# Performance work log

Measured on AMD Instinct MI355X. Metric: run time of the kernel, lower is better.

Reference implementation:

```python
import jax, jax.numpy as jnp
import numpy as np

H = 256   # hidden_size
L = 6     # num_layers
IN = 128  # input_size
B = 128   # batch
T = 512   # seq_len


def setup_inputs() -> dict:
    key = jax.random.key(0)
    ks = jax.random.split(key, 9)
    s = 1.0 / np.sqrt(H)  # PyTorch LSTM init: U(-1/sqrt(H), 1/sqrt(H))
    x = jax.random.normal(ks[0], (B, T, IN), jnp.float32)
    h0 = jax.random.normal(ks[1], (L, B, H), jnp.float32)
    c0 = jax.random.normal(ks[2], (L, B, H), jnp.float32)
    w_ih0 = jax.random.uniform(ks[3], (4 * H, IN), jnp.float32, -s, s)
    w_ih = jax.random.uniform(ks[4], (L - 1, 4 * H, H), jnp.float32, -s, s)
    w_hh = jax.random.uniform(ks[5], (L, 4 * H, H), jnp.float32, -s, s)
    b_ih = jax.random.uniform(ks[6], (L, 4 * H), jnp.float32, -s, s)
    b_hh = jax.random.uniform(ks[7], (L, 4 * H), jnp.float32, -s, s)
    return {"x": x, "h0": h0, "c0": c0, "w_ih0": w_ih0, "w_ih": w_ih,
            "w_hh": w_hh, "b_ih": b_ih, "b_hh": b_hh}


def _lstm_layer(x, h0, c0, w_ih, w_hh, b):
    """One unidirectional LSTM layer. x: [B,T,Din] -> outputs [B,T,H], (hT, cT)."""
    # Precompute input contribution for all timesteps at once: [B,T,4H]
    xg = jnp.einsum('btd,gd->btg', x, w_ih) + b

    def step(carry, g_t):
        h, c = carry
        g = g_t + h @ w_hh.T  # [B,4H]
        i, f, gc, o = jnp.split(g, 4, axis=-1)  # PyTorch gate order i,f,g,o
        i = jax.nn.sigmoid(i)
        f = jax.nn.sigmoid(f)
        o = jax.nn.sigmoid(o)
        gc = jnp.tanh(gc)
        c = f * c + i * gc
        h = o * jnp.tanh(c)
        return (h, c), h

    (hT, cT), ys = jax.lax.scan(step, (h0, c0), jnp.swapaxes(xg, 0, 1))
    return jnp.swapaxes(ys, 0, 1), hT, cT


def reference(x, h0, c0, w_ih0, w_ih, w_hh, b_ih, b_hh):
    # Stacked 6-layer LSTM; fc / noop linear in the original is dead code.
    # Original returns state[0] (final hidden states, [L,B,H]) as float32.
    hs = []
    inp = x
    for l in range(L):
        wih_l = w_ih0 if l == 0 else w_ih[l - 1]
        b_l = b_ih[l] + b_hh[l]
        inp, hT, _ = _lstm_layer(inp, h0[l], c0[l], wih_l, w_hh[l], b_l)
        hs.append(hT)
    return jnp.stack(hs).astype(jnp.float32)  # [L, B, H]
```

## Files before the change

kernel.cpp:

```cpp
#include <hip/hip_runtime.h>

#define NLAYER 6
#define NB     128
#define NT     512
#define DIN    128
#define NH     256
#define NBLK   192
#define SLOT_U64 (NB*NH/4)

typedef __attribute__((ext_vector_type(8))) short short8;
typedef __attribute__((ext_vector_type(4))) float f32x4;
typedef unsigned long long u64;

__device__ __forceinline__ unsigned f2bf2(float lo, float hi){
  unsigned a = __float_as_uint(lo), b = __float_as_uint(hi);
  a = (a + 0x7fffu + ((a>>16)&1u)) >> 16;
  b = (b + 0x7fffu + ((b>>16)&1u)) >> 16;
  return a | (b<<16);
}
__device__ __forceinline__ u64 f2bf4(float a, float b, float c, float d){
  return (u64)f2bf2(a,b) | ((u64)f2bf2(c,d) << 32);
}
__device__ __forceinline__ short8 pack16(u64 lo, u64 hi){
  union { u64 u[2]; short8 v; } w; w.u[0]=lo; w.u[1]=hi; return w.v;
}
__device__ __forceinline__ short8 ld8f_frag(const float* p){
  f32x4 a = *(const f32x4*)p;
  f32x4 b = *(const f32x4*)(p+4);
  return pack16(f2bf4(a[0],a[1],a[2],a[3]), f2bf4(b[0],b[1],b[2],b[3]));
}

__device__ __forceinline__ float sigmf(float v){ return 1.0f/(1.0f + __expf(-v)); }
__device__ __forceinline__ float tanhfast(float v){
  v = fminf(fmaxf(v, -15.0f), 15.0f);
  float e = __expf(2.0f*v);
  return (e - 1.0f)/(e + 1.0f);
}

__device__ __forceinline__ int ld_flag(const int* p){
  return __hip_atomic_load(p, __ATOMIC_RELAXED, __HIP_MEMORY_SCOPE_AGENT);
}
__device__ __forceinline__ void st_flag(int* p, int v){
  __hip_atomic_store(p, v, __ATOMIC_RELAXED, __HIP_MEMORY_SCOPE_AGENT);
}
__device__ __forceinline__ u64 ring_ld(const u64* p){
  return __hip_atomic_load(p, __ATOMIC_RELAXED, __HIP_MEMORY_SCOPE_AGENT);
}
__device__ __forceinline__ void ring_st(u64* p, u64 v){
  __hip_atomic_store(p, v, __ATOMIC_RELAXED, __HIP_MEMORY_SCOPE_AGENT);
}

__device__ __forceinline__ void poll2(const int* tH, int needH,
                                      const int* tX, int needX, int lane){
  const int* tp = nullptr; int need = 0;
  if (lane < 16)               { tp = tH + lane;        need = needH; }
  else if (tX && lane < 32)    { tp = tX + (lane - 16); need = needX; }
  int guard = 0;
  for (;;){
    int v = tp ? ld_flag(tp) : 0x7fffffff;
    if (__ballot(v >= need) == ~0ull) break;
    __builtin_amdgcn_s_sleep(1);
    if (++guard > (1<<22)) break;
  }
  asm volatile("" ::: "memory");
}

__device__ __forceinline__ void stage_plane(const u64* __restrict__ src,
                                            u64* __restrict__ dst, int wv, int lane){
  const int r = lane >> 4, c = lane & 15;
  const u64* p = src + (size_t)(wv*4 + r)*64 + c*4;
  u64 v0 = ring_ld(p), v1 = ring_ld(p+1), v2 = ring_ld(p+2), v3 = ring_ld(p+3);
  u64* d = dst + (wv*4 + r)*66 + c*4;
  d[0] = v0; d[1] = v1; d[2] = v2; d[3] = v3;
}
__device__ __forceinline__ short8 lds_frag(const u64* __restrict__ buf, int row, int off){
  return *(const short8*)((const short*)buf + row*264 + off);
}

template<int NKX>
__device__ __forceinline__ void lstm_run(
    const float* __restrict__ x,  const float* __restrict__ h0,
    const float* __restrict__ c0, const float* __restrict__ wx,
    const float* __restrict__ wh, const float* __restrict__ bi,
    const float* __restrict__ bh, float* __restrict__ out,
    int* __restrict__ tags, int* __restrict__ acks,
    u64* __restrict__ ring, u64 (*ldsb)[1056],
    int Wv, int l, int bg, int s, int wv, int lane)
{
  constexpr int KIT  = NKX + 8;
  constexpr int KX   = NKX*32;
  constexpr bool HASX = (NKX == 8);
  const int l15  = lane & 15;
  const int quad = lane >> 4;
  const int bloc = bg*16 + l15;
  const int jcol = s*16 + quad*4;
  const int Wm   = Wv - 1;

  short8 A[4][KIT];
  #pragma unroll
  for (int q = 0; q < 4; ++q){
    const float* wrow_x = wx + (size_t)(q*NH + s*16 + l15)*KX;
    const float* wrow_h = wh + (size_t)(q*NH + s*16 + l15)*NH;
    #pragma unroll
    for (int kt = 0; kt < KIT; ++kt){
      int k0 = kt*32 + quad*8;
      A[q][kt] = (k0 < KX) ? ld8f_frag(wrow_x + k0)
                           : ld8f_frag(wrow_h + (k0 - KX));
    }
  }

  f32x4 bsv[4];
  #pragma unroll
  for (int q = 0; q < 4; ++q){
    f32x4 a = *(const f32x4*)(bi + q*NH + jcol);
    f32x4 b = *(const f32x4*)(bh + q*NH + jcol);
    bsv[q] = a + b;
  }
  float cc[4];
  {
    f32x4 cv = *(const f32x4*)(c0 + ((size_t)l*NB + bloc)*NH + jcol);
    cc[0]=cv[0]; cc[1]=cv[1]; cc[2]=cv[2]; cc[3]=cv[3];
  }

  int* tagOwn   = tags + (l*8 + bg)*16;
  const int* tagPrev = HASX ? tags + ((l-1)*8 + bg)*16 : nullptr;
  const int* ackOwn  = acks + (l*8 + bg)*16;
  int* ackPrevW = HASX ? acks + ((l-1)*8 + bg)*16 + s : nullptr;
  const u64* ringPrev = HASX ? ring + (size_t)(l-1)*Wv*SLOT_U64 : nullptr;
  u64*       ringOwn  = ring + (size_t)l*Wv*SLOT_U64;
  const bool lastL = (l == NLAYER-1);
  const bool wrap  = (Wv < NT);
  int ackmin = 0;

  for (int t = 0; t < NT; ++t){
    const int slot  = t & Wm;
    const int pslot = (t-1) & Wm;

    if (wrap && !lastL && t >= Wv){
      const int need = t - Wv + 1;
      if (ackmin < need){
        int v = 0, guard = 0;
        for (;;){
          v = (lane < 16) ? ld_flag(ackOwn + lane) : 0x7fffffff;
          if (__ballot(v >= need) == ~0ull) break;
          __builtin_amdgcn_s_sleep(1);
          if (++guard > (1<<22)) break;
        }
        int m = v;
        #pragma unroll
        for (int o = 8; o; o >>= 1) m = min(m, __shfl_xor(m, o));
        ackmin = __shfl(m, 0);
      }
    }

    short8 Bx[NKX];
    if constexpr (!HASX){
      const float* px = x + ((size_t)bloc*NT + t)*DIN + quad*8;
      #pragma unroll
      for (int k = 0; k < NKX; ++k) Bx[k] = ld8f_frag(px + k*32);
    }

    poll2(tagOwn, t, tagPrev, t+1, lane);

    u64* ldsX = ldsb[(t&1)*2 + 0];
    u64* ldsH = ldsb[(t&1)*2 + 1];
    if constexpr (HASX)
      stage_plane(ringPrev + (size_t)slot*SLOT_U64 + (size_t)bg*16*64, ldsX, wv, lane);
    if (t > 0)
      stage_plane(ringOwn + (size_t)pslot*SLOT_U64 + (size_t)bg*16*64, ldsH, wv, lane);
    __syncthreads();

    if (HASX && wrap && ((t & 7) == 7) && lane == 0) st_flag(ackPrevW, t+1);

    if constexpr (HASX){
      #pragma unroll
      for (int k = 0; k < NKX; ++k) Bx[k] = lds_frag(ldsX, l15, quad*8 + k*32);
    }
    short8 Bh[8];
    if (t == 0){
      const float* ph = h0 + ((size_t)l*NB + bloc)*NH + quad*8;
      #pragma unroll
      for (int k = 0; k < 8; ++k) Bh[k] = ld8f_frag(ph + k*32);
    } else {
      #pragma unroll
      for (int k = 0; k < 8; ++k) Bh[k] = lds_frag(ldsH, l15, quad*8 + k*32);
    }

    f32x4 a0 = {0,0,0,0}, a1 = {0,0,0,0}, a2 = {0,0,0,0}, a3 = {0,0,0,0};
    #pragma unroll
    for (int k = 0; k < NKX; ++k){
      a0 = __builtin_amdgcn_mfma_f32_16x16x32_bf16(A[0][k], Bx[k], a0, 0, 0, 0);
      a1 = __builtin_amdgcn_mfma_f32_16x16x32_bf16(A[1][k], Bx[k], a1, 0, 0, 0);
      a2 = __builtin_amdgcn_mfma_f32_16x16x32_bf16(A[2][k], Bx[k], a2, 0, 0, 0);
      a3 = __builtin_amdgcn_mfma_f32_16x16x32_bf16(A[3][k], Bx[k], a3, 0, 0, 0);
    }
    #pragma unroll
    for (int k = 0; k < 8; ++k){
      a0 = __builtin_amdgcn_mfma_f32_16x16x32_bf16(A[0][NKX+k], Bh[k], a0, 0, 0, 0);
      a1 = __builtin_amdgcn_mfma_f32_16x16x32_bf16(A[1][NKX+k], Bh[k], a1, 0, 0, 0);
      a2 = __builtin_amdgcn_mfma_f32_16x16x32_bf16(A[2][NKX+k], Bh[k], a2, 0, 0, 0);
      a3 = __builtin_amdgcn_mfma_f32_16x16x32_bf16(A[3][NKX+k], Bh[k], a3, 0, 0, 0);
    }

    float hv[4];
    #pragma unroll
    for (int r = 0; r < 4; ++r){
      float ig = sigmf(a0[r] + bsv[0][r]);
      float fg = sigmf(a1[r] + bsv[1][r]);
      float gv = tanhfast(a2[r] + bsv[2][r]);
      float og = sigmf(a3[r] + bsv[3][r]);
      float cn = fg*cc[r] + ig*gv;
      cc[r] = cn;
      hv[r] = og * tanhfast(cn);
    }

    ring_st(ringOwn + (size_t)slot*SLOT_U64 + (size_t)bloc*64 + s*4 + quad,
            f2bf4(hv[0], hv[1], hv[2], hv[3]));
    if (t == NT-1){
      f32x4 ov; ov[0]=hv[0]; ov[1]=hv[1]; ov[2]=hv[2]; ov[3]=hv[3];
      *(f32x4*)(out + ((size_t)l*NB + bloc)*NH + jcol) = ov;
    }
    asm volatile("s_waitcnt vmcnt(0)" ::: "memory");
    if (lane == 0) st_flag(tagOwn + s, t+1);
  }
}

__global__ __launch_bounds__(256, 1)
void lstm_pipe(const float* __restrict__ x,   const float* __restrict__ h0,
               const float* __restrict__ c0,  const float* __restrict__ wih0,
               const float* __restrict__ wih, const float* __restrict__ whh,
               const float* __restrict__ bih, const float* __restrict__ bhh,
               float* __restrict__ out, int* __restrict__ tags,
               int* __restrict__ acks, u64* __restrict__ ring, int Wv)
{
  __shared__ u64 ldsb[4][1056];
  const int bid  = blockIdx.x;
  const int bg   = bid & 7;
  const int j    = bid >> 3;
  const int l    = j >> 2;
  const int b    = j & 3;
  const int lane = threadIdx.x & 63;
  const int wv   = threadIdx.x >> 6;
  const int s    = b*4 + wv;

  if (l == 0)
    lstm_run<4>(x, h0, c0, wih0, whh, bih, bhh,
                out, tags, acks, ring, ldsb, Wv, 0, bg, s, wv, lane);
  else
    lstm_run<8>(x, h0, c0,
                wih + (size_t)(l-1)*(4*NH*NH),
                whh + (size_t)l*(4*NH*NH),
                bih + (size_t)l*(4*NH),
                bhh + (size_t)l*(4*NH),
                out, tags, acks, ring, ldsb, Wv, l, bg, s, wv, lane);
}

extern "C" void kernel_launch(void* const* d_in, const int* in_sizes, int n_in,
                              void* d_out, int out_size, void* d_ws, size_t ws_size,
                              hipStream_t stream)
{
  (void)in_sizes; (void)n_in; (void)out_size;
  const float* x    = (const float*)d_in[0];
  const float* h0   = (const float*)d_in[1];
  const float* c0   = (const float*)d_in[2];
  const float* wih0 = (const float*)d_in[3];
  const float* wih  = (const float*)d_in[4];
  const float* whh  = (const float*)d_in[5];
  const float* bih  = (const float*)d_in[6];
  const float* bhh  = (const float*)d_in[7];

  int Wv = NT;
  size_t ringB;
  for (;;){
    ringB = (size_t)NLAYER*Wv*SLOT_U64*8;
    if (8192 + ringB <= ws_size || Wv <= 32) break;
    Wv >>= 1;
  }

  int* tags = (int*)d_ws;
  int* acks = (int*)((char*)d_ws + 4096);
  u64* ring = (u64*)((char*)d_ws + 8192);

  (void)hipMemsetAsync(d_ws, 0, 8192, stream);
  hipLaunchKernelGGL(lstm_pipe, dim3(NBLK), dim3(256), 0, stream,
                     x, h0, c0, wih0, wih, whh, bih, bhh,
                     (float*)d_out, tags, acks, ring, Wv);
}
```

Measured before the change: 2.289 ms.

## Embed timestep tags in ring data words to replace separate flag polling

Each bf16 hidden value is now stored in a 32-bit word whose low 16 bits carry the timestep tag. Consumers poll the data itself until every tag matches, then strip the tags into LDS. This removes the separate tag-flag store, the vmcnt(0) wait before it, and the flag-then-data double round trip on every step. In exchange the ring traffic doubles, the ring window shrinks to 32 slots (so ack-based backpressure now runs), and the whole ring must be memset before each launch.

```diff
diff --git a/kernel.cpp b/kernel.cpp
--- a/kernel.cpp
+++ b/kernel.cpp
@@ -6,7 +6,7 @@
 #define DIN    128
 #define NH     256
 #define NBLK   192
-#define SLOT_U64 (NB*NH/4)
+#define TSLOT_U64 (NB*NH/2)
 
 typedef __attribute__((ext_vector_type(8))) short short8;
 typedef __attribute__((ext_vector_type(4))) float f32x4;
@@ -50,31 +50,16 @@
   __hip_atomic_store(p, v, __ATOMIC_RELAXED, __HIP_MEMORY_SCOPE_AGENT);
 }
 
-__device__ __forceinline__ void poll2(const int* tH, int needH,
-                                      const int* tX, int needX, int lane){
-  const int* tp = nullptr; int need = 0;
-  if (lane < 16)               { tp = tH + lane;        need = needH; }
-  else if (tX && lane < 32)    { tp = tX + (lane - 16); need = needX; }
-  int guard = 0;
-  for (;;){
-    int v = tp ? ld_flag(tp) : 0x7fffffff;
-    if (__ballot(v >= need) == ~0ull) break;
-    __builtin_amdgcn_s_sleep(1);
-    if (++guard > (1<<22)) break;
-  }
-  asm volatile("" ::: "memory");
-}
-
-__device__ __forceinline__ void stage_plane(const u64* __restrict__ src,
-                                            u64* __restrict__ dst, int wv, int lane){
-  const int r = lane >> 4, c = lane & 15;
-  const u64* p = src + (size_t)(wv*4 + r)*64 + c*4;
-  u64 v0 = ring_ld(p), v1 = ring_ld(p+1), v2 = ring_ld(p+2), v3 = ring_ld(p+3);
-  u64* d = dst + (wv*4 + r)*66 + c*4;
-  d[0] = v0; d[1] = v1; d[2] = v2; d[3] = v3;
-}
-__device__ __forceinline__ short8 lds_frag(const u64* __restrict__ buf, int row, int off){
-  return *(const short8*)((const short*)buf + row*264 + off);
+__device__ __forceinline__ unsigned tagw(float f, unsigned tag){
+  unsigned a = __float_as_uint(f);
+  return ((a + 0x7fffu + ((a>>16)&1u)) & 0xffff0000u) | tag;
+}
+__device__ __forceinline__ unsigned strip2(u64 q){
+  return __builtin_amdgcn_perm((unsigned)(q>>32), (unsigned)q, 0x07060302u);
+}
+
+__device__ __forceinline__ short8 lds_frag(const unsigned* __restrict__ buf, int row, int soff){
+  return *(const short8*)((const short*)buf + row*264 + soff);
 }
 
 template<int NKX>
@@ -83,8 +68,7 @@
     const float* __restrict__ c0, const float* __restrict__ wx,
     const float* __restrict__ wh, const float* __restrict__ bi,
     const float* __restrict__ bh, float* __restrict__ out,
-    int* __restrict__ tags, int* __restrict__ acks,
-    u64* __restrict__ ring, u64 (*ldsb)[1056],
+    int* __restrict__ acks, u64* __restrict__ ring, unsigned (*ldsb)[2112],
     int Wv, int l, int bg, int s, int wv, int lane)
 {
   constexpr int KIT  = NKX + 8;
@@ -122,15 +106,15 @@
     cc[0]=cv[0]; cc[1]=cv[1]; cc[2]=cv[2]; cc[3]=cv[3];
   }
 
-  int* tagOwn   = tags + (l*8 + bg)*16;
-  const int* tagPrev = HASX ? tags + ((l-1)*8 + bg)*16 : nullptr;
-  const int* ackOwn  = acks + (l*8 + bg)*16;
+  const int* ackOwn = acks + (l*8 + bg)*16;
   int* ackPrevW = HASX ? acks + ((l-1)*8 + bg)*16 + s : nullptr;
-  const u64* ringPrev = HASX ? ring + (size_t)(l-1)*Wv*SLOT_U64 : nullptr;
-  u64*       ringOwn  = ring + (size_t)l*Wv*SLOT_U64;
+  const u64* ringPrev = HASX ? ring + (size_t)(l-1)*Wv*TSLOT_U64 : nullptr;
+  u64*       ringOwn  = ring + (size_t)l*Wv*TSLOT_U64;
   const bool lastL = (l == NLAYER-1);
   const bool wrap  = (Wv < NT);
   int ackmin = 0;
+
+  const int sbase = wv*512 + lane*2;
 
   for (int t = 0; t < NT; ++t){
     const int slot  = t & Wm;
@@ -160,14 +144,60 @@
       for (int k = 0; k < NKX; ++k) Bx[k] = ld8f_frag(px + k*32);
     }
 
-    poll2(tagOwn, t, tagPrev, t+1, lane);
-
-    u64* ldsX = ldsb[(t&1)*2 + 0];
-    u64* ldsH = ldsb[(t&1)*2 + 1];
-    if constexpr (HASX)
-      stage_plane(ringPrev + (size_t)slot*SLOT_U64 + (size_t)bg*16*64, ldsX, wv, lane);
-    if (t > 0)
-      stage_plane(ringOwn + (size_t)pslot*SLOT_U64 + (size_t)bg*16*64, ldsH, wv, lane);
+    const u64* srcX = HASX ? ringPrev + (size_t)slot*TSLOT_U64 + bg*2048 : nullptr;
+    const u64* srcH = (t > 0) ? ringOwn + (size_t)pslot*TSLOT_U64 + bg*2048 : nullptr;
+    unsigned* ldsX = ldsb[(t&1)*2 + 0];
+    unsigned* ldsH = ldsb[(t&1)*2 + 1];
+    u64 qx[8], qh[8];
+    {
+      bool okx = !HASX, okh = (srcH == nullptr);
+      const u64 tx2 = (u64)(unsigned)(t+1) * 0x0000000100000001ull;
+      const u64 th2 = (u64)(unsigned)t     * 0x0000000100000001ull;
+      int guard = 0;
+      while (!(okx & okh)){
+        if (!okx){
+          #pragma unroll
+          for (int c = 0; c < 4; ++c){
+            qx[c*2]   = ring_ld(srcX + sbase + c*128);
+            qx[c*2+1] = ring_ld(srcX + sbase + c*128 + 1);
+          }
+        }
+        if (!okh){
+          #pragma unroll
+          for (int c = 0; c < 4; ++c){
+            qh[c*2]   = ring_ld(srcH + sbase + c*128);
+            qh[c*2+1] = ring_ld(srcH + sbase + c*128 + 1);
+          }
+        }
+        if (!okx){
+          u64 m = 0;
+          #pragma unroll
+          for (int i = 0; i < 8; ++i) m |= qx[i] ^ tx2;
+          okx = (__ballot(((unsigned)(m | (m>>32)) & 0xffffu) == 0u) == ~0ull);
+        }
+        if (!okh){
+          u64 m = 0;
+          #pragma unroll
+          for (int i = 0; i < 8; ++i) m |= qh[i] ^ th2;
+          okh = (__ballot(((unsigned)(m | (m>>32)) & 0xffffu) == 0u) == ~0ull);
+        }
+        if (okx & okh) break;
+        __builtin_amdgcn_s_sleep(1);
+        if (++guard > (1<<20)) break;
+      }
+    }
+    if constexpr (HASX){
+      #pragma unroll
+      for (int c = 0; c < 4; ++c)
+        *(u64*)(ldsX + (wv*4+c)*132 + lane*2) =
+            (u64)strip2(qx[c*2]) | ((u64)strip2(qx[c*2+1]) << 32);
+    }
+    if (srcH){
+      #pragma unroll
+      for (int c = 0; c < 4; ++c)
+        *(u64*)(ldsH + (wv*4+c)*132 + lane*2) =
+            (u64)strip2(qh[c*2]) | ((u64)strip2(qh[c*2+1]) << 32);
+    }
     __syncthreads();
 
     if (HASX && wrap && ((t & 7) == 7) && lane == 0) st_flag(ackPrevW, t+1);
@@ -214,14 +244,14 @@
       hv[r] = og * tanhfast(cn);
     }
 
-    ring_st(ringOwn + (size_t)slot*SLOT_U64 + (size_t)bloc*64 + s*4 + quad,
-            f2bf4(hv[0], hv[1], hv[2], hv[3]));
+    u64* hp = ringOwn + (size_t)slot*TSLOT_U64 + (size_t)bloc*128 + s*8 + quad*2;
+    const unsigned otag = (unsigned)(t+1);
+    ring_st(hp,     (u64)tagw(hv[0], otag) | ((u64)tagw(hv[1], otag) << 32));
+    ring_st(hp + 1, (u64)tagw(hv[2], otag) | ((u64)tagw(hv[3], otag) << 32));
     if (t == NT-1){
       f32x4 ov; ov[0]=hv[0]; ov[1]=hv[1]; ov[2]=hv[2]; ov[3]=hv[3];
       *(f32x4*)(out + ((size_t)l*NB + bloc)*NH + jcol) = ov;
     }
-    asm volatile("s_waitcnt vmcnt(0)" ::: "memory");
-    if (lane == 0) st_flag(tagOwn + s, t+1);
   }
 }
 
@@ -230,10 +260,10 @@
                const float* __restrict__ c0,  const float* __restrict__ wih0,
                const float* __restrict__ wih, const float* __restrict__ whh,
                const float* __restrict__ bih, const float* __restrict__ bhh,
-               float* __restrict__ out, int* __restrict__ tags,
-               int* __restrict__ acks, u64* __restrict__ ring, int Wv)
+               float* __restrict__ out, int* __restrict__ acks,
+               u64* __restrict__ ring, int Wv)
 {
-  __shared__ u64 ldsb[4][1056];
+  __shared__ unsigned ldsb[4][2112];
   const int bid  = blockIdx.x;
   const int bg   = bid & 7;
   const int j    = bid >> 3;
@@ -245,14 +275,14 @@
 
   if (l == 0)
     lstm_run<4>(x, h0, c0, wih0, whh, bih, bhh,
-                out, tags, acks, ring, ldsb, Wv, 0, bg, s, wv, lane);
+                out, acks, ring, ldsb, Wv, 0, bg, s, wv, lane);
   else
     lstm_run<8>(x, h0, c0,
                 wih + (size_t)(l-1)*(4*NH*NH),
                 whh + (size_t)l*(4*NH*NH),
                 bih + (size_t)l*(4*NH),
                 bhh + (size_t)l*(4*NH),
-                out, tags, acks, ring, ldsb, Wv, l, bg, s, wv, lane);
+                out, acks, ring, ldsb, Wv, l, bg, s, wv, lane);
 }
 
 extern "C" void kernel_launch(void* const* d_in, const int* in_sizes, int n_in,
@@ -269,20 +299,19 @@
   const float* bih  = (const float*)d_in[6];
   const float* bhh  = (const float*)d_in[7];
 
-  int Wv = NT;
+  int Wv = 32;
   size_t ringB;
   for (;;){
-    ringB = (size_t)NLAYER*Wv*SLOT_U64*8;
-    if (8192 + ringB <= ws_size || Wv <= 32) break;
+    ringB = (size_t)NLAYER*Wv*TSLOT_U64*8;
+    if (8192 + ringB <= ws_size || Wv <= 8) break;
     Wv >>= 1;
   }
 
-  int* tags = (int*)d_ws;
-  int* acks = (int*)((char*)d_ws + 4096);
+  int* acks = (int*)d_ws;
   u64* ring = (u64*)((char*)d_ws + 8192);
 
-  (void)hipMemsetAsync(d_ws, 0, 8192, stream);
+  (void)hipMemsetAsync(d_ws, 0, 8192 + ringB, stream);
   hipLaunchKernelGGL(lstm_pipe, dim3(NBLK), dim3(256), 0, stream,
                      x, h0, c0, wih0, wih, whh, bih, bhh,
-                     (float*)d_out, tags, acks, ring, Wv);
-}
+                     (float*)d_out, acks, ring, Wv);
+}
```

Measured after the change: 2.091 ms. -8.7%, faster.
